# Performance work log

Hardware: AMD Instinct MI355X
Metric: run time of the kernel (lower is better)

Reference implementation:

```python
import jax, jax.numpy as jnp
import numpy as np

N, M, B = 2048, 2048, 1
D, H, DQK, DV = 1024, 16, 64, 64
OFFSET = 0
PARAM_SCALE = 0.02  # keeps logits in a sane range (original uses plain randn)


def setup_inputs() -> dict:
    key = jax.random.key(0)
    ks = jax.random.split(key, 7)
    return {
        "x_q": jax.random.normal(ks[0], (N, B, D), jnp.float32),
        "x_kv": jax.random.normal(ks[1], (M, B, D), jnp.float32),
        "to_q": jax.random.normal(ks[2], (DQK, H, D), jnp.float32) * PARAM_SCALE,
        "to_k": jax.random.normal(ks[3], (DQK, H, D), jnp.float32) * PARAM_SCALE,
        "to_v": jax.random.normal(ks[4], (DV, H, D), jnp.float32) * PARAM_SCALE,
        "to_out": jax.random.normal(ks[5], (D, DV, H), jnp.float32) * PARAM_SCALE,
        "for_pos_enc": jax.random.normal(ks[6], (DQK, H, D), jnp.float32) * PARAM_SCALE,
    }


def _sincos(n, m, offset, d_x_kv, dtype):
    # relative distances i - j + offset range over [offset-(m-1), offset+(n-1)]
    r = jnp.arange(offset - (m - 1), offset + (n - 1) + 1, dtype=dtype)  # [R], R=n+m-1
    inv_freq = 1.0 / (10000.0 ** (jnp.arange(0.0, d_x_kv, 2.0, dtype=dtype) / d_x_kv))
    phases = r[:, None] * inv_freq[None, :]  # [R, d/2]
    return jnp.concatenate([jnp.sin(phases), jnp.cos(phases)], axis=-1)  # [R, d]


def reference(x_q, x_kv, to_q, to_k, to_v, to_out, for_pos_enc):
    n, b, _ = x_q.shape
    m = x_kv.shape[0]
    # q: [n, d_qk, b, h]
    q = jnp.einsum('dhb,nab->ndah', to_q, x_q)
    # content logits: [n, m, b, h]
    k = jnp.einsum('dhc,mac->mdah', to_k, x_kv)
    content = jnp.einsum('ndah,mdah->nmah', q, k)
    # relative positional encoding (same math as pos_enc[dists - min] then einsum,
    # but logits computed per relative position then gathered -> no [n,m,d,h] blowup)
    sincos = _sincos(n, m, OFFSET, x_kv.shape[-1], x_q.dtype)  # [R, d_x_kv]
    pe_rel = jnp.einsum('dhb,rb->rdh', for_pos_enc, sincos)    # [R, d_qk, h]
    pl_rel = jnp.einsum('ndah,rdh->nrah', q, pe_rel)            # [n, R, b, h]
    idx = jnp.arange(n)[:, None] - jnp.arange(m)[None, :] + (m - 1)  # dists - dists.min()
    position = pl_rel[jnp.arange(n)[:, None], idx]               # [n, m, b, h]
    logits = content + position
    # causal mask: True above diagonal shifted by 1+offset
    mask = jnp.triu(jnp.ones((n, m), bool), 1 + OFFSET)
    logits = jnp.where(mask[:, :, None, None], -jnp.inf, logits)
    weights = jax.nn.softmax(logits, axis=1)                     # softmax over m
    v = jnp.einsum('chb,mab->mach', to_v, x_kv)                  # [m, b, dv, h]
    ctx = jnp.einsum('nmah,mach->nach', weights, v)              # [n, b, dv, h]
    out = jnp.einsum('dch,nach->nad', to_out, ctx)               # [n, b, d]
    return out
```

## Files before the change

### kernel.cpp

```cpp
#include <hip/hip_runtime.h>
#include <hip/hip_bf16.h>

#define N_Q   2048
#define M_KV  2048
#define DIM   1024
#define NH    16
#define DHEAD 64
#define KDIM  1024
#define PEROWS 2112
#define PEBUF  2176

typedef __attribute__((ext_vector_type(8))) __bf16 bf16x8;
typedef __attribute__((ext_vector_type(4))) float  f32x4;

typedef __attribute__((address_space(1))) const unsigned char gbyte_t;
typedef __attribute__((address_space(3))) unsigned char lbyte_t;

__device__ __forceinline__ unsigned short f2bf(float f) {
  union { float f; unsigned u; } v; v.f = f;
  unsigned u = v.u;
  u = u + 0x7fffu + ((u >> 16) & 1u);
  return (unsigned short)(u >> 16);
}

#define PREP_A 524288
#define PREP_B 1048576
#define PREP_C 2097152
#define PREP_D 2359296
#define PREP_E 2916352
__global__ __launch_bounds__(256) void prep_kernel(
    const float* __restrict__ x_q, const float* __restrict__ x_kv,
    const float* __restrict__ to_q, const float* __restrict__ to_k,
    const float* __restrict__ to_v, const float* __restrict__ to_pe,
    const float* __restrict__ to_out,
    unsigned short* __restrict__ xq_bf, unsigned short* __restrict__ xkv_bf,
    unsigned short* __restrict__ wq_bf, unsigned short* __restrict__ wkv_bf,
    unsigned short* __restrict__ wp_bf, unsigned short* __restrict__ wo_bf,
    unsigned short* __restrict__ sc_bf) {
  int gid = blockIdx.x * 256 + threadIdx.x;
  if (gid < PREP_B) {
    const float* src = (gid < PREP_A) ? x_q : x_kv;
    unsigned short* dst = (gid < PREP_A) ? xq_bf : xkv_bf;
    int e4 = (gid < PREP_A ? gid : gid - PREP_A) * 4;
    float4 v = *(const float4*)(src + e4);
    ushort4 o = { f2bf(v.x), f2bf(v.y), f2bf(v.z), f2bf(v.w) };
    *(ushort4*)(dst + e4) = o;
  } else if (gid < PREP_C) {
    int e = gid - PREP_B;
    int which = e >> 18, inner = e & 262143;
    int e4 = inner * 4;
    int j = e4 >> 10, b = e4 & 1023;
    int d = j & 63, h = j >> 6;
    const float* w = (which == 0) ? to_q : (which == 1) ? to_k : (which == 2) ? to_v : to_pe;
    unsigned short* o = (which == 0) ? wq_bf : (which == 1) ? wkv_bf
                       : (which == 2) ? (wkv_bf + (size_t)DIM * DIM) : wp_bf;
    float4 v = *(const float4*)(w + (size_t)(d * NH + h) * DIM + b);
    ushort4 u = { f2bf(v.x), f2bf(v.y), f2bf(v.z), f2bf(v.w) };
    *(ushort4*)(o + e4) = u;
  } else if (gid < PREP_D) {
    int e4 = (gid - PREP_C) * 4;
    int dd = e4 >> 10, jc = e4 & 1023;
    int c = jc & 63, h = jc >> 6;
    const float* base = to_out + (size_t)(dd * DHEAD + c) * NH + h;
    ushort4 u = { f2bf(base[0]), f2bf(base[16]), f2bf(base[32]), f2bf(base[48]) };
    *(ushort4*)(wo_bf + e4) = u;
  } else if (gid < PREP_E) {
    int e = gid - PREP_D;
    int r = e >> 8, t8 = e & 255;
    float ph0base = (float)(r - 63);
    unsigned short ss[2], cc[2];
    #pragma unroll
    for (int i = 0; i < 2; ++i) {
      int k2 = t8 * 2 + i;
      float invf = __expf((float)k2 * (-9.210340371976184f / 512.0f));
      float s, c;
      __sincosf(ph0base * invf, &s, &c);
      ss[i] = f2bf(s); cc[i] = f2bf(c);
    }
    unsigned short* row = sc_bf + (size_t)r * DIM;
    *(unsigned int*)(row + t8 * 2)       = (unsigned)ss[0] | ((unsigned)ss[1] << 16);
    *(unsigned int*)(row + t8 * 2 + 512) = (unsigned)cc[0] | ((unsigned)cc[1] << 16);
  }
}

__global__ __launch_bounds__(256) void gemm_in_kernel(
    const unsigned short* __restrict__ xq, const unsigned short* __restrict__ xkv,
    const unsigned short* __restrict__ sc,
    const unsigned short* __restrict__ wq, const unsigned short* __restrict__ wkv,
    const unsigned short* __restrict__ wp,
    unsigned short* __restrict__ qout, unsigned short* __restrict__ kout,
    unsigned short* __restrict__ vtout, unsigned short* __restrict__ peout) {
  int bid = blockIdx.x;
  const unsigned short *A, *B; unsigned short *C1, *C2;
  int Mr, maxBrow, mode, ax, by;
  if (bid < 256)      { int t = bid;       ax = t & 15; by = t >> 4; A = xq;  B = wq;  C1 = qout;  C2 = nullptr; Mr = N_Q;    maxBrow = DIM - 1;     mode = 1; }
  else if (bid < 768) { int t = bid - 256; ax = t & 15; by = t >> 4; A = xkv; B = wkv; C1 = kout;  C2 = vtout;   Mr = M_KV;   maxBrow = 2 * DIM - 1; mode = 3; }
  else                { int t = bid - 768; ax = t % 17; by = t / 17; A = sc;  B = wp;  C1 = peout; C2 = nullptr; Mr = PEROWS; maxBrow = DIM - 1;     mode = 1; }

  __shared__ unsigned short As[2][128][64];
  __shared__ unsigned short Bs[2][64][64];
  int tid  = threadIdx.x;
  int wave = tid >> 6, lane = tid & 63;
  int g = lane >> 4, r16 = lane & 15;
  int arow0 = ax * 128;
  int brow0 = by * 64;
  int amax  = Mr - 1;

  auto stage = [&](int buf, int kt) {
    #pragma unroll
    for (int n = 0; n < 4; ++n) {
      int seg  = wave * 4 + n;
      int rloc = seg * 8 + (lane >> 3);
      int cbyte = ((lane & 7) << 4) ^ ((rloc & 7) << 4);
      int grow = min(arow0 + rloc, amax);
      const unsigned short* gp = A + (size_t)grow * KDIM + kt + (cbyte >> 1);
      __builtin_amdgcn_global_load_lds((gbyte_t*)(const void*)gp,
                                       (lbyte_t*)(void*)&As[buf][seg * 8][0], 16, 0, 0);
    }
    #pragma unroll
    for (int n = 0; n < 2; ++n) {
      int seg  = wave * 2 + n;
      int rloc = seg * 8 + (lane >> 3);
      int cbyte = ((lane & 7) << 4) ^ ((rloc & 7) << 4);
      int grow = min(brow0 + rloc, maxBrow);
      const unsigned short* gp = B + (size_t)grow * KDIM + kt + (cbyte >> 1);
      __builtin_amdgcn_global_load_lds((gbyte_t*)(const void*)gp,
                                       (lbyte_t*)(void*)&Bs[buf][seg * 8][0], 16, 0, 0);
    }
  };

  f32x4 acc[2][4];
  #pragma unroll
  for (int i = 0; i < 2; ++i)
    #pragma unroll
    for (int j = 0; j < 4; ++j) acc[i][j] = (f32x4){0,0,0,0};

  stage(0, 0);
  asm volatile("s_waitcnt vmcnt(0)" ::: "memory");
  __syncthreads();

  int buf = 0;
  for (int t = 0; t < 16; ++t) {
    if (t < 15) stage(buf ^ 1, (t + 1) * 64);

    bf16x8 af[2][2], bfr[4][2];
    #pragma unroll
    for (int i = 0; i < 2; ++i)
      #pragma unroll
      for (int kk = 0; kk < 2; ++kk) {
        int r = wave * 32 + i * 16 + r16;
        int cb = ((kk << 6) | (g << 4)) ^ ((r & 7) << 4);
        af[i][kk] = *(const bf16x8*)((const char*)&As[buf][r][0] + cb);
      }
    #pragma unroll
    for (int j = 0; j < 4; ++j)
      #pragma unroll
      for (int kk = 0; kk < 2; ++kk) {
        int r = j * 16 + r16;
        int cb = ((kk << 6) | (g << 4)) ^ ((r & 7) << 4);
        bfr[j][kk] = *(const bf16x8*)((const char*)&Bs[buf][r][0] + cb);
      }
    __builtin_amdgcn_s_setprio(1);
    #pragma unroll
    for (int kk = 0; kk < 2; ++kk)
      #pragma unroll
      for (int i = 0; i < 2; ++i)
        #pragma unroll
        for (int j = 0; j < 4; ++j)
          acc[i][j] = __builtin_amdgcn_mfma_f32_16x16x32_bf16(af[i][kk], bfr[j][kk], acc[i][j], 0, 0, 0);
    __builtin_amdgcn_s_setprio(0);

    if (t < 15) {
      asm volatile("s_waitcnt vmcnt(0)" ::: "memory");
      __syncthreads();
      buf ^= 1;
    }
  }

  #pragma unroll
  for (int i = 0; i < 2; ++i)
    #pragma unroll
    for (int j = 0; j < 4; ++j)
      #pragma unroll
      for (int rr = 0; rr < 4; ++rr) {
        int row = arow0 + wave * 32 + i * 16 + g * 4 + rr;
        int col = brow0 + j * 16 + r16;
        float v = acc[i][j][rr];
        if (mode == 1) {
          if (row < Mr) C1[(size_t)row * 1024 + col] = f2bf(v);
        } else {
          if (col < 1024) C1[(size_t)row * 1024 + col] = f2bf(v);
          else            C2[(size_t)(col - 1024) * M_KV + row] = f2bf(v);
        }
      }
}

__global__ __launch_bounds__(256) void gemm_out_kernel(
    const unsigned short* __restrict__ A, const unsigned short* __restrict__ B,
    float* __restrict__ C1) {
  __shared__ unsigned short As[2][128][64];
  __shared__ unsigned short Bs[2][64][64];
  int tid  = threadIdx.x;
  int wave = tid >> 6, lane = tid & 63;
  int g = lane >> 4, r16 = lane & 15;
  int arow0 = blockIdx.x * 128;
  int brow0 = blockIdx.y * 64;

  auto stage = [&](int buf, int kt) {
    #pragma unroll
    for (int n = 0; n < 4; ++n) {
      int seg  = wave * 4 + n;
      int rloc = seg * 8 + (lane >> 3);
      int cbyte = ((lane & 7) << 4) ^ ((rloc & 7) << 4);
      const unsigned short* gp = A + (size_t)(arow0 + rloc) * KDIM + kt + (cbyte >> 1);
      __builtin_amdgcn_global_load_lds((gbyte_t*)(const void*)gp,
                                       (lbyte_t*)(void*)&As[buf][seg * 8][0], 16, 0, 0);
    }
    #pragma unroll
    for (int n = 0; n < 2; ++n) {
      int seg  = wave * 2 + n;
      int rloc = seg * 8 + (lane >> 3);
      int cbyte = ((lane & 7) << 4) ^ ((rloc & 7) << 4);
      const unsigned short* gp = B + (size_t)(brow0 + rloc) * KDIM + kt + (cbyte >> 1);
      __builtin_amdgcn_global_load_lds((gbyte_t*)(const void*)gp,
                                       (lbyte_t*)(void*)&Bs[buf][seg * 8][0], 16, 0, 0);
    }
  };

  f32x4 acc[2][4];
  #pragma unroll
  for (int i = 0; i < 2; ++i)
    #pragma unroll
    for (int j = 0; j < 4; ++j) acc[i][j] = (f32x4){0,0,0,0};

  stage(0, 0);
  asm volatile("s_waitcnt vmcnt(0)" ::: "memory");
  __syncthreads();

  int buf = 0;
  for (int t = 0; t < 16; ++t) {
    if (t < 15) stage(buf ^ 1, (t + 1) * 64);
    bf16x8 af[2][2], bfr[4][2];
    #pragma unroll
    for (int i = 0; i < 2; ++i)
      #pragma unroll
      for (int kk = 0; kk < 2; ++kk) {
        int r = wave * 32 + i * 16 + r16;
        int cb = ((kk << 6) | (g << 4)) ^ ((r & 7) << 4);
        af[i][kk] = *(const bf16x8*)((const char*)&As[buf][r][0] + cb);
      }
    #pragma unroll
    for (int j = 0; j < 4; ++j)
      #pragma unroll
      for (int kk = 0; kk < 2; ++kk) {
        int r = j * 16 + r16;
        int cb = ((kk << 6) | (g << 4)) ^ ((r & 7) << 4);
        bfr[j][kk] = *(const bf16x8*)((const char*)&Bs[buf][r][0] + cb);
      }
    __builtin_amdgcn_s_setprio(1);
    #pragma unroll
    for (int kk = 0; kk < 2; ++kk)
      #pragma unroll
      for (int i = 0; i < 2; ++i)
        #pragma unroll
        for (int j = 0; j < 4; ++j)
          acc[i][j] = __builtin_amdgcn_mfma_f32_16x16x32_bf16(af[i][kk], bfr[j][kk], acc[i][j], 0, 0, 0);
    __builtin_amdgcn_s_setprio(0);
    if (t < 15) {
      asm volatile("s_waitcnt vmcnt(0)" ::: "memory");
      __syncthreads();
      buf ^= 1;
    }
  }

  #pragma unroll
  for (int i = 0; i < 2; ++i)
    #pragma unroll
    for (int j = 0; j < 4; ++j)
      #pragma unroll
      for (int rr = 0; rr < 4; ++rr) {
        int row = arow0 + wave * 32 + i * 16 + g * 4 + rr;
        int col = brow0 + j * 16 + r16;
        C1[(size_t)row * 1024 + col] = acc[i][j][rr];
      }
}

__global__ __launch_bounds__(256, 2) void attn_mfma_kernel(
    const unsigned short* __restrict__ qb, const unsigned short* __restrict__ kb,
    const unsigned short* __restrict__ vt, const unsigned short* __restrict__ pe,
    unsigned short* __restrict__ ctx, float* __restrict__ part) {
  int ord  = (int)blockIdx.x;
  int h    = ord & 15;
  int widx = 79 - (ord >> 4);
  int b, c;
  if (widx < 8)       { b = widx;                                  c = 0; }
  else if (widx < 24) { int t2 = widx - 8;  b = 8  + (t2 >> 1);    c = t2 & 1; }
  else if (widx < 48) { int t2 = widx - 24; int q3 = t2 / 3; b = 16 + q3; c = t2 - 3 * q3; }
  else                { int t2 = widx - 48; b = 24 + (t2 >> 2);    c = t2 & 3; }
  int n0   = b * 64;
  int nc   = (b < 8) ? 1 : (b >> 3) + 1;
  int t0   = c * 8;
  int tend = min(t0 + 8, b + 1);

  int wave = threadIdx.x >> 6;
  int lane = threadIdx.x & 63;
  int g    = lane >> 4;
  int r16  = lane & 15;

  __shared__ unsigned short Ks[2][64][64];
  __shared__ unsigned short Vs[2][64][64];
  __shared__ unsigned short PEs[2][128][64];
  __shared__ unsigned short W_lds[4][16][72];

  const unsigned short* qrow = qb + (size_t)(n0 + wave * 16 + r16) * DIM + h * 64 + g * 8;
  bf16x8 aq0 = *(const bf16x8*)(qrow);
  bf16x8 aq1 = *(const bf16x8*)(qrow + 32);

  union { unsigned short u[8]; bf16x8 v; } one_u;
  #pragma unroll
  for (int i = 0; i < 8; ++i) one_u.u[i] = 0x3F80;
  bf16x8 ones = one_u.v;

  f32x4 acc[4] = {{0,0,0,0},{0,0,0,0},{0,0,0,0},{0,0,0,0}};
  f32x4 lacc = {0,0,0,0};

  auto stage = [&](int bufn, int tilen) {
    int m0n = tilen * 64;
    int prb = n0 - m0n;
    #pragma unroll
    for (int n = 0; n < 2; ++n) {
      int seg  = wave * 2 + n;
      int rloc = seg * 8 + (lane >> 3);
      int cbyte = ((lane & 7) << 4) ^ ((rloc & 7) << 4);
      const unsigned short* gpk = kb + (size_t)(m0n + rloc) * KDIM + h * 64 + (cbyte >> 1);
      __builtin_amdgcn_global_load_lds((gbyte_t*)(const void*)gpk,
                                       (lbyte_t*)(void*)&Ks[bufn][seg * 8][0], 16, 0, 0);
      const unsigned short* gpv = vt + (size_t)(h * 64 + rloc) * M_KV + m0n + (cbyte >> 1);
      __builtin_amdgcn_global_load_lds((gbyte_t*)(const void*)gpv,
                                       (lbyte_t*)(void*)&Vs[bufn][seg * 8][0], 16, 0, 0);
    }
    #pragma unroll
    for (int n = 0; n < 4; ++n) {
      int seg  = wave * 4 + n;
      int rloc = seg * 8 + (lane >> 3);
      int cbyte = ((lane & 7) << 4) ^ ((rloc & 7) << 4);
      const unsigned short* gpp = pe + (size_t)(prb + rloc) * KDIM + h * 64 + (cbyte >> 1);
      __builtin_amdgcn_global_load_lds((gbyte_t*)(const void*)gpp,
                                       (lbyte_t*)(void*)&PEs[bufn][seg * 8][0], 16, 0, 0);
    }
  };

  int srcl[4]; bool hi_sel[4];
  #pragma unroll
  for (int rr = 0; rr < 4; ++rr) {
    srcl[rr]   = (g << 4) | ((g * 4 + rr + 63 - r16) & 15);
    hi_sel[rr] = (g * 4 + rr) > r16;
  }
  int sw = (r16 & 7) << 4;

  stage(0, t0);
  asm volatile("s_waitcnt vmcnt(0)" ::: "memory");
  __syncthreads();

  int buf = 0;
  for (int tile = t0; tile < tend; ++tile) {
    int m0 = tile * 64;
    if (tile + 1 < tend) stage(buf ^ 1, tile + 1);

    f32x4 s[4];
    __builtin_amdgcn_s_setprio(1);
    #pragma unroll
    for (int ct = 0; ct < 4; ++ct) {
      const char* kbase = (const char*)&Ks[buf][ct * 16 + r16][0];
      bf16x8 k0 = *(const bf16x8*)(kbase + (((g << 4)) ^ sw));
      bf16x8 k1 = *(const bf16x8*)(kbase + ((64 | (g << 4)) ^ sw));
      f32x4 z = {0,0,0,0};
      z = __builtin_amdgcn_mfma_f32_16x16x32_bf16(aq0, k0, z, 0, 0, 0);
      z = __builtin_amdgcn_mfma_f32_16x16x32_bf16(aq1, k1, z, 0, 0, 0);
      s[ct] = z;
    }

    f32x4 z2[5];
    #pragma unroll
    for (int cp = 0; cp < 5; ++cp) {
      const char* pbase = (const char*)&PEs[buf][wave * 16 + cp * 16 + r16][0];
      bf16x8 p0 = *(const bf16x8*)(pbase + (((g << 4)) ^ sw));
      bf16x8 p1 = *(const bf16x8*)(pbase + ((64 | (g << 4)) ^ sw));
      f32x4 z = {0,0,0,0};
      z = __builtin_amdgcn_mfma_f32_16x16x32_bf16(aq0, p0, z, 0, 0, 0);
      z = __builtin_amdgcn_mfma_f32_16x16x32_bf16(aq1, p1, z, 0, 0, 0);
      z2[cp] = z;
    }
    __builtin_amdgcn_s_setprio(0);

    bool diag = (m0 == n0);
    #pragma unroll
    for (int ct = 0; ct < 4; ++ct) {
      #pragma unroll
      for (int rr = 0; rr < 4; ++rr) {
        float vhi = __shfl(z2[4 - ct][rr], srcl[rr], 64);
        float vlo = __shfl(z2[3 - ct][rr], srcl[rr], 64);
        float p   = hi_sel[rr] ? vhi : vlo;
        int il = g * 4 + rr;
        int it = wave * 16 + il;
        int jt = ct * 16 + r16;
        float val = s[ct][rr] + p;
        if (diag && jt > it) val = -1e30f;
        s[ct][rr] = __expf(val);
      }
    }

    #pragma unroll
    for (int ct = 0; ct < 4; ++ct)
      #pragma unroll
      for (int rr = 0; rr < 4; ++rr)
        W_lds[wave][g * 4 + rr][ct * 16 + r16] = f2bf(s[ct][rr]);
    bf16x8 aw0 = *(const bf16x8*)(&W_lds[wave][r16][g * 8]);
    bf16x8 aw1 = *(const bf16x8*)(&W_lds[wave][r16][g * 8 + 32]);

    __builtin_amdgcn_s_setprio(1);
    #pragma unroll
    for (int ct = 0; ct < 4; ++ct) {
      const char* vbase = (const char*)&Vs[buf][ct * 16 + r16][0];
      bf16x8 v0 = *(const bf16x8*)(vbase + (((g << 4)) ^ sw));
      bf16x8 v1 = *(const bf16x8*)(vbase + ((64 | (g << 4)) ^ sw));
      f32x4 a = acc[ct];
      a = __builtin_amdgcn_mfma_f32_16x16x32_bf16(aw0, v0, a, 0, 0, 0);
      a = __builtin_amdgcn_mfma_f32_16x16x32_bf16(aw1, v1, a, 0, 0, 0);
      acc[ct] = a;
    }
    lacc = __builtin_amdgcn_mfma_f32_16x16x32_bf16(aw0, ones, lacc, 0, 0, 0);
    lacc = __builtin_amdgcn_mfma_f32_16x16x32_bf16(aw1, ones, lacc, 0, 0, 0);
    __builtin_amdgcn_s_setprio(0);

    asm volatile("s_waitcnt vmcnt(0)" ::: "memory");
    __syncthreads();
    buf ^= 1;
  }

  if (nc == 1) {
    #pragma unroll
    for (int rr = 0; rr < 4; ++rr) {
      float inv = 1.0f / lacc[rr];
      #pragma unroll
      for (int ct = 0; ct < 4; ++ct) {
        int row = n0 + wave * 16 + g * 4 + rr;
        ctx[(size_t)row * DIM + h * 64 + ct * 16 + r16] = f2bf(acc[ct][rr] * inv);
      }
    }
  } else {
    float* slot = part + ((size_t)((b - 8) * 16 + h) * 4 + c) * (64 * 68);
    #pragma unroll
    for (int ct = 0; ct < 4; ++ct)
      #pragma unroll
      for (int rr = 0; rr < 4; ++rr) {
        int row = wave * 16 + g * 4 + rr;
        slot[row * 68 + ct * 16 + r16] = acc[ct][rr];
      }
    if (r16 == 0) {
      #pragma unroll
      for (int rr = 0; rr < 4; ++rr) {
        int row = wave * 16 + g * 4 + rr;
        slot[row * 68 + 64] = lacc[rr];
      }
    }
  }
}

__global__ __launch_bounds__(256) void combine_kernel(const float* __restrict__ part,
                                                      unsigned short* __restrict__ ctx) {
  int bb = blockIdx.x;
  int h  = blockIdx.y;
  int b  = bb + 8;
  int nc = (b >> 3) + 1;
  int t  = threadIdx.x;
  int row = t >> 2, q = t & 3;
  const float* base = part + ((size_t)(bb * 16 + h) * 4) * (64 * 68) + row * 68;
  float lstar = 0.0f;
  for (int c2 = 0; c2 < nc; ++c2) lstar += base[c2 * 4352 + 64];
  float inv = 1.0f / lstar;
  for (int cc = 0; cc < 16; ++cc) {
    int col = q * 16 + cc;
    float o = 0.0f;
    for (int c2 = 0; c2 < nc; ++c2) o += base[c2 * 4352 + col];
    ctx[(size_t)(b * 64 + row) * DIM + h * 64 + col] = f2bf(o * inv);
  }
}

extern "C" void kernel_launch(void* const* d_in, const int* in_sizes, int n_in,
                              void* d_out, int out_size, void* d_ws, size_t ws_size,
                              hipStream_t stream) {
  const float* x_q    = (const float*)d_in[0];
  const float* x_kv   = (const float*)d_in[1];
  const float* to_q   = (const float*)d_in[2];
  const float* to_k   = (const float*)d_in[3];
  const float* to_v   = (const float*)d_in[4];
  const float* to_out = (const float*)d_in[5];
  const float* to_pe  = (const float*)d_in[6];

  char* ws = (char*)d_ws;
  size_t off = 0;
  auto alloc = [&](size_t bytes) -> char* {
    char* p = ws + off;
    off += (bytes + 255) & ~(size_t)255;
    return p;
  };

  unsigned short* xq_bf  = (unsigned short*)alloc((size_t)N_Q  * DIM * 2);
  unsigned short* xkv_bf = (unsigned short*)alloc((size_t)M_KV * DIM * 2);
  unsigned short* wq_bf  = (unsigned short*)alloc((size_t)DIM * DIM * 2);
  unsigned short* wkv_bf = (unsigned short*)alloc((size_t)2 * DIM * DIM * 2);
  unsigned short* wp_bf  = (unsigned short*)alloc((size_t)DIM * DIM * 2);
  unsigned short* wo_bf  = (unsigned short*)alloc((size_t)DIM * DIM * 2);
  unsigned short* sc_bf  = (unsigned short*)alloc((size_t)PEBUF * DIM * 2);
  unsigned short* q_bf   = (unsigned short*)alloc((size_t)N_Q  * DIM * 2);
  unsigned short* k_bf   = (unsigned short*)alloc((size_t)M_KV * DIM * 2);
  unsigned short* vt_bf  = (unsigned short*)alloc((size_t)DIM * M_KV * 2);
  unsigned short* pe_bf  = (unsigned short*)alloc((size_t)PEBUF * DIM * 2);
  unsigned short* ctx_bf = (unsigned short*)alloc((size_t)N_Q * DIM * 2);
  float*          part   = (float*)alloc((size_t)24 * 16 * 4 * 64 * 68 * 4);

  prep_kernel<<<11392, 256, 0, stream>>>(x_q, x_kv, to_q, to_k, to_v, to_pe, to_out,
                                         xq_bf, xkv_bf, wq_bf, wkv_bf, wp_bf, wo_bf, sc_bf);

  gemm_in_kernel<<<1040, 256, 0, stream>>>(xq_bf, xkv_bf, sc_bf, wq_bf, wkv_bf, wp_bf,
                                           q_bf, k_bf, vt_bf, pe_bf);

  attn_mfma_kernel<<<1280, 256, 0, stream>>>(q_bf, k_bf, vt_bf, pe_bf, ctx_bf, part);
  combine_kernel<<<dim3(24, NH), 256, 0, stream>>>(part, ctx_bf);

  gemm_out_kernel<<<dim3(16, 16), 256, 0, stream>>>(ctx_bf, wo_bf, (float*)d_out);
}
```

Baseline: 130.3 us.

## Software-pipeline attention loop by computing next tile's logits after the barrier

The QK and positional-logit MFMAs move into a lambda that runs for the next tile right after the end-of-iteration barrier, rather than at the start of each iteration. Softmax and PV for the current tile then run on logits computed ahead of time, and the final barrier and wait are skipped on the last tile. The aim is to let one tile's logit MFMAs interleave with the previous tile's exp and PV work across waves. The trade-off is that the global loads for the following tile now overlap only softmax and PV, not the logit MFMAs, and more registers stay live across iterations.

```diff
diff --git a/kernel.cpp b/kernel.cpp
--- a/kernel.cpp
+++ b/kernel.cpp
@@ -90,7 +90,7 @@
     const unsigned short* __restrict__ wp,
     unsigned short* __restrict__ qout, unsigned short* __restrict__ kout,
     unsigned short* __restrict__ vtout, unsigned short* __restrict__ peout) {
-  int bid = blockIdx.x;
+  int bid = (int)blockIdx.x;
   const unsigned short *A, *B; unsigned short *C1, *C2;
   int Mr, maxBrow, mode, ax, by;
   if (bid < 256)      { int t = bid;       ax = t & 15; by = t >> 4; A = xq;  B = wq;  C1 = qout;  C2 = nullptr; Mr = N_Q;    maxBrow = DIM - 1;     mode = 1; }
@@ -358,53 +358,56 @@
   }
   int sw = (r16 & 7) << 4;
 
-  stage(0, t0);
-  asm volatile("s_waitcnt vmcnt(0)" ::: "memory");
-  __syncthreads();
-
-  int buf = 0;
-  for (int tile = t0; tile < tend; ++tile) {
-    int m0 = tile * 64;
-    if (tile + 1 < tend) stage(buf ^ 1, tile + 1);
-
-    f32x4 s[4];
+  f32x4 sA[4], zA[5];
+  auto compute = [&](int bufc) {
     __builtin_amdgcn_s_setprio(1);
     #pragma unroll
     for (int ct = 0; ct < 4; ++ct) {
-      const char* kbase = (const char*)&Ks[buf][ct * 16 + r16][0];
+      const char* kbase = (const char*)&Ks[bufc][ct * 16 + r16][0];
       bf16x8 k0 = *(const bf16x8*)(kbase + (((g << 4)) ^ sw));
       bf16x8 k1 = *(const bf16x8*)(kbase + ((64 | (g << 4)) ^ sw));
       f32x4 z = {0,0,0,0};
       z = __builtin_amdgcn_mfma_f32_16x16x32_bf16(aq0, k0, z, 0, 0, 0);
       z = __builtin_amdgcn_mfma_f32_16x16x32_bf16(aq1, k1, z, 0, 0, 0);
-      s[ct] = z;
-    }
-
-    f32x4 z2[5];
+      sA[ct] = z;
+    }
     #pragma unroll
     for (int cp = 0; cp < 5; ++cp) {
-      const char* pbase = (const char*)&PEs[buf][wave * 16 + cp * 16 + r16][0];
+      const char* pbase = (const char*)&PEs[bufc][wave * 16 + cp * 16 + r16][0];
       bf16x8 p0 = *(const bf16x8*)(pbase + (((g << 4)) ^ sw));
       bf16x8 p1 = *(const bf16x8*)(pbase + ((64 | (g << 4)) ^ sw));
       f32x4 z = {0,0,0,0};
       z = __builtin_amdgcn_mfma_f32_16x16x32_bf16(aq0, p0, z, 0, 0, 0);
       z = __builtin_amdgcn_mfma_f32_16x16x32_bf16(aq1, p1, z, 0, 0, 0);
-      z2[cp] = z;
+      zA[cp] = z;
     }
     __builtin_amdgcn_s_setprio(0);
+  };
+
+  stage(0, t0);
+  asm volatile("s_waitcnt vmcnt(0)" ::: "memory");
+  __syncthreads();
+  compute(0);
+
+  int buf = 0;
+  for (int tile = t0; tile < tend; ++tile) {
+    int m0 = tile * 64;
+    bool more = (tile + 1 < tend);
+    if (more) stage(buf ^ 1, tile + 1);
 
     bool diag = (m0 == n0);
+    f32x4 s[4];
     #pragma unroll
     for (int ct = 0; ct < 4; ++ct) {
       #pragma unroll
       for (int rr = 0; rr < 4; ++rr) {
-        float vhi = __shfl(z2[4 - ct][rr], srcl[rr], 64);
-        float vlo = __shfl(z2[3 - ct][rr], srcl[rr], 64);
+        float vhi = __shfl(zA[4 - ct][rr], srcl[rr], 64);
+        float vlo = __shfl(zA[3 - ct][rr], srcl[rr], 64);
         float p   = hi_sel[rr] ? vhi : vlo;
         int il = g * 4 + rr;
         int it = wave * 16 + il;
         int jt = ct * 16 + r16;
-        float val = s[ct][rr] + p;
+        float val = sA[ct][rr] + p;
         if (diag && jt > it) val = -1e30f;
         s[ct][rr] = __expf(val);
       }
@@ -433,9 +436,13 @@
     lacc = __builtin_amdgcn_mfma_f32_16x16x32_bf16(aw1, ones, lacc, 0, 0, 0);
     __builtin_amdgcn_s_setprio(0);
 
-    asm volatile("s_waitcnt vmcnt(0)" ::: "memory");
-    __syncthreads();
-    buf ^= 1;
+    if (more) {
+      asm volatile("s_waitcnt vmcnt(0)" ::: "memory");
+      __builtin_amdgcn_s_barrier();
+      __builtin_amdgcn_sched_barrier(0);
+      compute(buf ^ 1);
+      buf ^= 1;
+    }
   }
 
   if (nc == 1) {
```

After: 131.5 us. No clear change (+0.9%).
